# Performance work log

Measured on AMD Instinct MI355X. Metric: run time of the kernel, lower is better.

The kernel has to match this reference:

```python
import jax, jax.numpy as jnp
import numpy as np

N = 50000      # nodes
E = 800000     # edges
XS = 64        # x_size
ES = 32        # edge_attr dim (in_size = XS + ES = 96)
OUT = 64       # out_size
H = 128        # hidden_size
EPS = 1e-5


def _lin_init(k, fan_in, fan_out):
    s = 1.0 / np.sqrt(fan_in)
    kw, kb = jax.random.split(k)
    w = jax.random.uniform(kw, (fan_in, fan_out), minval=-s, maxval=s, dtype=jnp.float32)
    b = jax.random.uniform(kb, (fan_out,), minval=-s, maxval=s, dtype=jnp.float32)
    return w, b


def setup_inputs() -> dict:
    key = jax.random.key(0)
    ks = jax.random.split(key, 12)
    x = jax.random.normal(ks[0], (N, XS), dtype=jnp.float32)
    edge_index = jax.random.randint(ks[1], (2, E), 0, N, dtype=jnp.int64)
    edge_attr = jax.random.normal(ks[2], (E, ES), dtype=jnp.float32)
    u = jax.random.normal(ks[3], (1, 8), dtype=jnp.float32)
    batch = jnp.zeros((N,), dtype=jnp.int64)
    # MLP1: (96->128) LReLU (128->128) LReLU (128->64) LReLU LN(64)
    m1w0, m1b0 = _lin_init(ks[4], XS + ES, H)
    m1w1, m1b1 = _lin_init(ks[5], H, H)
    m1w2, m1b2 = _lin_init(ks[6], H, OUT)
    ln1_g = jnp.ones((OUT,), jnp.float32); ln1_b = jnp.zeros((OUT,), jnp.float32)
    # MLP2: (128->128) LReLU (128->128) LReLU (128->64) LReLU LN(64)
    m2w0, m2b0 = _lin_init(ks[7], XS + OUT, H)
    m2w1, m2b1 = _lin_init(ks[8], H, H)
    m2w2, m2b2 = _lin_init(ks[9], H, OUT)
    ln2_g = jnp.ones((OUT,), jnp.float32); ln2_b = jnp.zeros((OUT,), jnp.float32)
    return dict(x=x, edge_index=edge_index, edge_attr=edge_attr, u=u, batch=batch,
                m1w0=m1w0, m1b0=m1b0, m1w1=m1w1, m1b1=m1b1, m1w2=m1w2, m1b2=m1b2,
                ln1_g=ln1_g, ln1_b=ln1_b,
                m2w0=m2w0, m2b0=m2b0, m2w1=m2w1, m2b1=m2b1, m2w2=m2w2, m2b2=m2b2,
                ln2_g=ln2_g, ln2_b=ln2_b)


def _lrelu(v):
    return jax.nn.leaky_relu(v, 0.01)


def _layernorm(v, g, b):
    mu = jnp.mean(v, axis=-1, keepdims=True)
    var = jnp.mean(jnp.square(v - mu), axis=-1, keepdims=True)
    return (v - mu) * jax.lax.rsqrt(var + EPS) * g + b


def _mlp(h, w0, b0, w1, b1, w2, b2, g, bn):
    h = _lrelu(h @ w0 + b0)
    h = _lrelu(h @ w1 + b1)
    h = _lrelu(h @ w2 + b2)          # activate_last=True
    return _layernorm(h, g, bn)      # layer_norm=True


def reference(x, edge_index, edge_attr, u, batch,
              m1w0, m1b0, m1w1, m1b1, m1w2, m1b2, ln1_g, ln1_b,
              m2w0, m2b0, m2w1, m2b1, m2w2, m2b2, ln2_g, ln2_b):
    row, col = edge_index[0], edge_index[1]
    # gather source nodes, concat edge features -> per-edge MLP
    h = jnp.concatenate([x[row], edge_attr], axis=1)            # [E, 96]
    h = _mlp(h, m1w0, m1b0, m1w1, m1b1, m1w2, m1b2, ln1_g, ln1_b)  # [E, 64]
    # scatter_mean over destination nodes
    agg = jax.ops.segment_sum(h, col, num_segments=N)           # [N, 64]
    cnt = jax.ops.segment_sum(jnp.ones((E,), h.dtype), col, num_segments=N)
    agg = agg / jnp.maximum(cnt, 1.0)[:, None]
    # node update MLP
    h2 = jnp.concatenate([x, agg], axis=1)                      # [N, 128]
    return _mlp(h2, m2w0, m2b0, m2w1, m2b1, m2w2, m2b2, ln2_g, ln2_b)
```

## Files before the change

kernel.cpp:

```cpp
#include <hip/hip_runtime.h>


#define NNODES 50000
#define NEDGES 800000
#define NTILES_E 6250
#define NTILES_N 196

typedef __bf16 bf16;
typedef __bf16 __attribute__((ext_vector_type(4))) bf16x4;
typedef __bf16 __attribute__((ext_vector_type(8))) bf16x8;
typedef float __attribute__((ext_vector_type(4))) f32x4;

__device__ __forceinline__ f32x4 mfma_bf16(bf16x8 a, bf16x8 b, f32x4 c) {
    return __builtin_amdgcn_mfma_f32_16x16x32_bf16(a, b, c, 0, 0, 0);
}

__global__ void prep_weights(const float* __restrict__ w10, const float* __restrict__ w11,
                             const float* __restrict__ w12, const float* __restrict__ w20,
                             const float* __restrict__ w21, const float* __restrict__ w22,
                             bf16* __restrict__ img) {
    int idx = blockIdx.x * 256 + threadIdx.x;
    float f;
    if (idx < 13312) {
        int n = idx / 104, k = idx % 104;
        f = (k < 96) ? w10[k * 128 + n] : 0.0f;
    } else if (idx < 30720) {
        int t = idx - 13312; int n = t / 136, k = t % 136;
        f = (k < 128) ? w11[k * 128 + n] : 0.0f;
    } else if (idx < 39424) {
        int t = idx - 30720; int n = t / 136, k = t % 136;
        f = (k < 128) ? w12[k * 64 + n] : 0.0f;
    } else if (idx < 56832) {
        int t = idx - 39424; int n = t / 136, k = t % 136;
        f = (k < 128) ? w20[k * 128 + n] : 0.0f;
    } else if (idx < 74240) {
        int t = idx - 56832; int n = t / 136, k = t % 136;
        f = (k < 128) ? w21[k * 128 + n] : 0.0f;
    } else if (idx < 82944) {
        int t = idx - 74240; int n = t / 136, k = t % 136;
        f = (k < 128) ? w22[k * 64 + n] : 0.0f;
    } else {
        return;
    }
    img[idx] = (bf16)f;
}

__global__ void hist_kernel(const int* __restrict__ col, int* __restrict__ hist) {
    int i = blockIdx.x * 512 + threadIdx.x;
    if (i < NEDGES) {
        int d = col[i];
        if ((unsigned)d < (unsigned)NNODES) atomicAdd(hist + d, 1);
    }
}

__global__ void scanA(const int* __restrict__ hist, int* __restrict__ off,
                      int* __restrict__ csum) {
    __shared__ int sd[512];
    int t = threadIdx.x, i = blockIdx.x * 512 + t;
    int v = (i < NNODES) ? hist[i] : 0;
    sd[t] = v;
    __syncthreads();
    for (int o2 = 1; o2 < 512; o2 <<= 1) {
        int x = (t >= o2) ? sd[t - o2] : 0;
        __syncthreads();
        sd[t] += x;
        __syncthreads();
    }
    if (i < NNODES) off[i] = sd[t] - v;
    if (t == 511) csum[blockIdx.x] = sd[511];
}

__global__ void scanB(int* __restrict__ csum) {
    __shared__ int sd[128];
    int t = threadIdx.x;
    int v = (t < 98) ? csum[t] : 0;
    sd[t] = v;
    __syncthreads();
    for (int o2 = 1; o2 < 128; o2 <<= 1) {
        int x = (t >= o2) ? sd[t - o2] : 0;
        __syncthreads();
        sd[t] += x;
        __syncthreads();
    }
    if (t < 98) csum[t] = sd[t] - v;
}

__global__ void scanC(int* __restrict__ off, const int* __restrict__ csum) {
    int i = blockIdx.x * 512 + threadIdx.x;
    if (i < NNODES) off[i] += csum[blockIdx.x];
}

__global__ void scatter_kernel(const int* __restrict__ eidx, int* __restrict__ off,
                               int* __restrict__ perm, int* __restrict__ rdS) {
    int i = blockIdx.x * 512 + threadIdx.x;
    if (i < NEDGES) {
        int r = eidx[i], d = eidx[NEDGES + i];
        if ((unsigned)d < (unsigned)NNODES && (unsigned)r < (unsigned)NNODES) {
            int pos = atomicAdd(off + d, 1);
            if ((unsigned)pos < (unsigned)NEDGES) {
                perm[pos] = i;
                rdS[pos] = (int)(((unsigned)r & 0xFFFFu) | ((unsigned)d << 16));
            }
        }
    }
}

__global__ __launch_bounds__(256) void edge_mlp(
    const float* __restrict__ x, const int* __restrict__ perm,
    const int* __restrict__ rdS, const float* __restrict__ eattr,
    const bf16* __restrict__ wimg,
    const float* __restrict__ b0g, const float* __restrict__ b1g,
    const float* __restrict__ b2g, const float* __restrict__ lng,
    const float* __restrict__ lnb, float* __restrict__ agg) {
    __shared__ __align__(16) bf16 w1l[17408];
    __shared__ __align__(16) bf16 buf[128 * 136];
    __shared__ float bs[448];
    __shared__ int dstile[128];

    const int tid = threadIdx.x;
    {
        const uint4* src = (const uint4*)(wimg + 13312);
        uint4* dst = (uint4*)w1l;
        for (int i = tid; i < 2176; i += 256) dst[i] = src[i];
    }
    if (tid < 128) { bs[tid] = b0g[tid]; bs[128 + tid] = b1g[tid]; }
    else if (tid < 192) {
        int t = tid - 128;
        bs[256 + t] = b2g[t]; bs[320 + t] = lng[t]; bs[384 + t] = lnb[t];
    }
    __syncthreads();

    const int lane = tid & 63;
    const int wv = tid >> 6;
    const int col16 = lane & 15;
    const int quad = lane >> 4;

    float b0r[8], b1r[8], b2r[4], gr[4], br[4];
#pragma unroll
    for (int i = 0; i < 8; i++) { b0r[i] = bs[i * 16 + col16]; b1r[i] = bs[128 + i * 16 + col16]; }
#pragma unroll
    for (int i = 0; i < 4; i++) {
        b2r[i] = bs[256 + i * 16 + col16];
        gr[i] = bs[320 + i * 16 + col16];
        br[i] = bs[384 + i * 16 + col16];
    }

    const bf16* w0t = wimg;
    const bf16* w2t = wimg + 30720;

    const f32x4 vzero = {0.0f, 0.0f, 0.0f, 0.0f};
    const int r0 = wv * 32 + col16;
    const int rw = wv * 32 + quad * 4;
    const int el = tid >> 1, half = tid & 1;
    const int G = gridDim.x;

    int tile = blockIdx.x;

    float4 xr[8], er[4];
    unsigned cv;
    {
        int s = tile * 128 + el;
        cv = (unsigned)rdS[s];
        int ce = perm[s];
        int r = (int)(cv & 0xFFFFu); if (r >= NNODES) r = 0;
        if ((unsigned)ce >= (unsigned)NEDGES) ce = 0;
        const float4* xs = (const float4*)(x + (size_t)r * 64) + half * 8;
        const float4* es = (const float4*)(eattr + (size_t)ce * 32) + half * 4;
#pragma unroll
        for (int j = 0; j < 8; j++) xr[j] = xs[j];
#pragma unroll
        for (int j = 0; j < 4; j++) er[j] = es[j];
    }
    unsigned nv; int ne;
    {
        int t1 = tile + G;
        int s = (t1 < NTILES_E ? t1 * 128 : 0) + el;
        nv = (unsigned)rdS[s];
        ne = perm[s];
    }

    for (; tile < NTILES_E; tile += G) {
        {
            unsigned d = cv >> 16;
            if (half == 0) dstile[el] = (d < (unsigned)NNODES) ? (int)d : 0;
            bf16* arow = buf + el * 136;
#pragma unroll
            for (int j = 0; j < 8; j++) {
                float4 vv = xr[j];
                bf16x4 u = {(bf16)vv.x, (bf16)vv.y, (bf16)vv.z, (bf16)vv.w};
                *(bf16x4*)(arow + half * 32 + j * 4) = u;
            }
#pragma unroll
            for (int j = 0; j < 4; j++) {
                float4 vv = er[j];
                bf16x4 u = {(bf16)vv.x, (bf16)vv.y, (bf16)vv.z, (bf16)vv.w};
                *(bf16x4*)(arow + 64 + half * 16 + j * 4) = u;
            }
        }
        __syncthreads();

        {
            int t2 = tile + G;
            if (t2 < NTILES_E) {
                int r = (int)(nv & 0xFFFFu); if (r >= NNODES) r = 0;
                int e = ne; if ((unsigned)e >= (unsigned)NEDGES) e = 0;
                const float4* xs = (const float4*)(x + (size_t)r * 64) + half * 8;
                const float4* es = (const float4*)(eattr + (size_t)e * 32) + half * 4;
#pragma unroll
                for (int j = 0; j < 8; j++) xr[j] = xs[j];
#pragma unroll
                for (int j = 0; j < 4; j++) er[j] = es[j];
            }
        }
        unsigned pv; int pe;
        {
            int t3 = tile + 2 * G;
            int s = (t3 < NTILES_E ? t3 * 128 : 0) + el;
            pv = (unsigned)rdS[s];
            pe = perm[s];
        }

        f32x4 acc1[2][8];
#pragma unroll
        for (int mt = 0; mt < 2; mt++)
#pragma unroll
            for (int nt = 0; nt < 8; nt++) acc1[mt][nt] = vzero;
#pragma unroll
        for (int ks = 0; ks < 3; ks++) {
            bf16x8 a0 = *(const bf16x8*)(buf + r0 * 136 + ks * 32 + quad * 8);
            bf16x8 a1 = *(const bf16x8*)(buf + (r0 + 16) * 136 + ks * 32 + quad * 8);
#pragma unroll
            for (int nt = 0; nt < 8; nt++) {
                bf16x8 b = *(const bf16x8*)(w0t + (nt * 16 + col16) * 104 + ks * 32 + quad * 8);
                acc1[0][nt] = mfma_bf16(a0, b, acc1[0][nt]);
                acc1[1][nt] = mfma_bf16(a1, b, acc1[1][nt]);
            }
        }
#pragma unroll
        for (int mt = 0; mt < 2; mt++)
#pragma unroll
            for (int nt = 0; nt < 8; nt++)
#pragma unroll
                for (int rg = 0; rg < 4; rg++) {
                    float v = acc1[mt][nt][rg] + b0r[nt];
                    v = (v > 0.0f) ? v : 0.01f * v;
                    buf[(rw + mt * 16 + rg) * 136 + nt * 16 + col16] = (bf16)v;
                }

        bf16x8 a2[2][4];
#pragma unroll
        for (int mt = 0; mt < 2; mt++)
#pragma unroll
            for (int ks = 0; ks < 4; ks++)
                a2[mt][ks] = *(const bf16x8*)(buf + (r0 + mt * 16) * 136 + ks * 32 + quad * 8);
        f32x4 acc2[2][8];
#pragma unroll
        for (int mt = 0; mt < 2; mt++)
#pragma unroll
            for (int nt = 0; nt < 8; nt++) acc2[mt][nt] = vzero;
#pragma unroll
        for (int ks = 0; ks < 4; ks++) {
#pragma unroll
            for (int nt = 0; nt < 8; nt++) {
                bf16x8 b = *(const bf16x8*)(w1l + (nt * 16 + col16) * 136 + ks * 32 + quad * 8);
                acc2[0][nt] = mfma_bf16(a2[0][ks], b, acc2[0][nt]);
                acc2[1][nt] = mfma_bf16(a2[1][ks], b, acc2[1][nt]);
            }
        }
#pragma unroll
        for (int mt = 0; mt < 2; mt++)
#pragma unroll
            for (int nt = 0; nt < 8; nt++)
#pragma unroll
                for (int rg = 0; rg < 4; rg++) {
                    float v = acc2[mt][nt][rg] + b1r[nt];
                    v = (v > 0.0f) ? v : 0.01f * v;
                    buf[(rw + mt * 16 + rg) * 136 + nt * 16 + col16] = (bf16)v;
                }

        bf16x8 a3[2][4];
#pragma unroll
        for (int mt = 0; mt < 2; mt++)
#pragma unroll
            for (int ks = 0; ks < 4; ks++)
                a3[mt][ks] = *(const bf16x8*)(buf + (r0 + mt * 16) * 136 + ks * 32 + quad * 8);
        f32x4 acc3[2][4];
#pragma unroll
        for (int mt = 0; mt < 2; mt++)
#pragma unroll
            for (int nt = 0; nt < 4; nt++) acc3[mt][nt] = vzero;
#pragma unroll
        for (int ks = 0; ks < 4; ks++) {
#pragma unroll
            for (int nt = 0; nt < 4; nt++) {
                bf16x8 b = *(const bf16x8*)(w2t + (nt * 16 + col16) * 136 + ks * 32 + quad * 8);
                acc3[0][nt] = mfma_bf16(a3[0][ks], b, acc3[0][nt]);
                acc3[1][nt] = mfma_bf16(a3[1][ks], b, acc3[1][nt]);
            }
        }

        int drA[2][4];
#pragma unroll
        for (int mt = 0; mt < 2; mt++)
#pragma unroll
            for (int rg = 0; rg < 4; rg++) {
                int c = dstile[rw + mt * 16 + rg];
                drA[mt][rg] = ((unsigned)c < (unsigned)NNODES) ? c : 0;
            }
        __syncthreads();

#pragma unroll
        for (int mt = 0; mt < 2; mt++) {
            float vals[4][4];
            float s1[4] = {0.f, 0.f, 0.f, 0.f}, s2[4] = {0.f, 0.f, 0.f, 0.f};
#pragma unroll
            for (int nt = 0; nt < 4; nt++)
#pragma unroll
                for (int rg = 0; rg < 4; rg++) {
                    float v = acc3[mt][nt][rg] + b2r[nt];
                    v = (v > 0.0f) ? v : 0.01f * v;
                    vals[nt][rg] = v;
                    s1[rg] += v;
                    s2[rg] += v * v;
                }
#pragma unroll
            for (int off2 = 1; off2 < 16; off2 <<= 1) {
#pragma unroll
                for (int rg = 0; rg < 4; rg++) {
                    s1[rg] += __shfl_xor(s1[rg], off2);
                    s2[rg] += __shfl_xor(s2[rg], off2);
                }
            }
            float o[4][4];
#pragma unroll
            for (int rg = 0; rg < 4; rg++) {
                float mu = s1[rg] * 0.015625f;
                float var = s2[rg] * 0.015625f - mu * mu;
                float rstd = rsqrtf(var + 1e-5f);
#pragma unroll
                for (int nt = 0; nt < 4; nt++)
                    o[nt][rg] = (vals[nt][rg] - mu) * rstd * gr[nt] + br[nt];
            }
            float run0 = o[0][0], run1 = o[1][0], run2 = o[2][0], run3 = o[3][0];
            int cur = drA[mt][0];
#pragma unroll
            for (int rg = 1; rg < 4; rg++) {
                if (drA[mt][rg] != cur) {
                    float* dst = agg + (size_t)cur * 64 + col16;
                    atomicAdd(dst, run0); atomicAdd(dst + 16, run1);
                    atomicAdd(dst + 32, run2); atomicAdd(dst + 48, run3);
                    run0 = o[0][rg]; run1 = o[1][rg]; run2 = o[2][rg]; run3 = o[3][rg];
                    cur = drA[mt][rg];
                } else {
                    run0 += o[0][rg]; run1 += o[1][rg]; run2 += o[2][rg]; run3 += o[3][rg];
                }
            }
            float* dst = agg + (size_t)cur * 64 + col16;
            atomicAdd(dst, run0); atomicAdd(dst + 16, run1);
            atomicAdd(dst + 32, run2); atomicAdd(dst + 48, run3);
        }

        cv = nv; nv = pv; ne = pe;
    }
}

__global__ __launch_bounds__(512, 2) void node_mlp(
    const float* __restrict__ x, const float* __restrict__ agg,
    const int* __restrict__ hist, const bf16* __restrict__ wimg,
    const float* __restrict__ b0g, const float* __restrict__ b1g,
    const float* __restrict__ b2g, const float* __restrict__ lng,
    const float* __restrict__ lnb, float* __restrict__ out) {
    __shared__ __align__(16) bf16 wall[43520];
    __shared__ __align__(16) bf16 buf[256 * 136];
    __shared__ float bs[448];

    const int tid = threadIdx.x;
    {
        const uint4* src = (const uint4*)wimg;
        uint4* dst = (uint4*)wall;
        for (int i = tid; i < 5440; i += 512) dst[i] = src[i];
    }
    if (tid < 128) { bs[tid] = b0g[tid]; bs[128 + tid] = b1g[tid]; }
    else if (tid < 192) {
        int t = tid - 128;
        bs[256 + t] = b2g[t]; bs[320 + t] = lng[t]; bs[384 + t] = lnb[t];
    }
    __syncthreads();

    const int lane = tid & 63;
    const int wv = tid >> 6;
    const int col16 = lane & 15;
    const int quad = lane >> 4;

    float b0r[8], b1r[8], b2r[4], gr[4], br[4];
#pragma unroll
    for (int i = 0; i < 8; i++) { b0r[i] = bs[i * 16 + col16]; b1r[i] = bs[128 + i * 16 + col16]; }
#pragma unroll
    for (int i = 0; i < 4; i++) {
        b2r[i] = bs[256 + i * 16 + col16];
        gr[i] = bs[320 + i * 16 + col16];
        br[i] = bs[384 + i * 16 + col16];
    }

    const bf16* w0t = wall;
    const bf16* w1t = wall + 17408;
    const bf16* w2t = wall + 34816;

    const f32x4 vzero = {0.0f, 0.0f, 0.0f, 0.0f};
    const int r0 = wv * 32 + col16;
    const int rw = wv * 32 + quad * 4;
    const int el = tid >> 1, half = tid & 1;
    const int G = gridDim.x;

    int tile = blockIdx.x;
    if (tile >= NTILES_N) return;

    float4 xr[8], ar[8];
    int cc;
    {
        int i = tile * 256 + el;
        if (i >= NNODES) i = NNODES - 1;
        const float4* xs = (const float4*)(x + (size_t)i * 64) + half * 8;
        const float4* as = (const float4*)(agg + (size_t)i * 64) + half * 8;
#pragma unroll
        for (int j = 0; j < 8; j++) { xr[j] = xs[j]; ar[j] = as[j]; }
        cc = hist[i];
    }

    for (; tile < NTILES_N; tile += G) {
        const int nbase = tile * 256;
        {
            float inv = 1.0f / (float)(cc > 1 ? cc : 1);
            bf16* arow = buf + el * 136;
#pragma unroll
            for (int j = 0; j < 8; j++) {
                float4 v = xr[j];
                bf16x4 u = {(bf16)v.x, (bf16)v.y, (bf16)v.z, (bf16)v.w};
                *(bf16x4*)(arow + half * 32 + j * 4) = u;
            }
#pragma unroll
            for (int j = 0; j < 8; j++) {
                float4 v = ar[j];
                bf16x4 u = {(bf16)(v.x * inv), (bf16)(v.y * inv), (bf16)(v.z * inv), (bf16)(v.w * inv)};
                *(bf16x4*)(arow + 64 + half * 32 + j * 4) = u;
            }
        }
        __syncthreads();

        {
            int t2 = tile + G;
            if (t2 < NTILES_N) {
                int i = t2 * 256 + el;
                if (i >= NNODES) i = NNODES - 1;
                const float4* xs = (const float4*)(x + (size_t)i * 64) + half * 8;
                const float4* as = (const float4*)(agg + (size_t)i * 64) + half * 8;
#pragma unroll
                for (int j = 0; j < 8; j++) { xr[j] = xs[j]; ar[j] = as[j]; }
                cc = hist[i];
            }
        }

        f32x4 acc1[2][8];
#pragma unroll
        for (int mt = 0; mt < 2; mt++)
#pragma unroll
            for (int nt = 0; nt < 8; nt++) acc1[mt][nt] = vzero;
#pragma unroll
        for (int ks = 0; ks < 4; ks++) {
            bf16x8 a0 = *(const bf16x8*)(buf + r0 * 136 + ks * 32 + quad * 8);
            bf16x8 a1 = *(const bf16x8*)(buf + (r0 + 16) * 136 + ks * 32 + quad * 8);
#pragma unroll
            for (int nt = 0; nt < 8; nt++) {
                bf16x8 b = *(const bf16x8*)(w0t + (nt * 16 + col16) * 136 + ks * 32 + quad * 8);
                acc1[0][nt] = mfma_bf16(a0, b, acc1[0][nt]);
                acc1[1][nt] = mfma_bf16(a1, b, acc1[1][nt]);
            }
        }
#pragma unroll
        for (int mt = 0; mt < 2; mt++)
#pragma unroll
            for (int nt = 0; nt < 8; nt++)
#pragma unroll
                for (int rg = 0; rg < 4; rg++) {
                    float v = acc1[mt][nt][rg] + b0r[nt];
                    v = (v > 0.0f) ? v : 0.01f * v;
                    buf[(rw + mt * 16 + rg) * 136 + nt * 16 + col16] = (bf16)v;
                }

        bf16x8 a2[2][4];
#pragma unroll
        for (int mt = 0; mt < 2; mt++)
#pragma unroll
            for (int ks = 0; ks < 4; ks++)
                a2[mt][ks] = *(const bf16x8*)(buf + (r0 + mt * 16) * 136 + ks * 32 + quad * 8);
        f32x4 acc2[2][8];
#pragma unroll
        for (int mt = 0; mt < 2; mt++)
#pragma unroll
            for (int nt = 0; nt < 8; nt++) acc2[mt][nt] = vzero;
#pragma unroll
        for (int ks = 0; ks < 4; ks++) {
#pragma unroll
            for (int nt = 0; nt < 8; nt++) {
                bf16x8 b = *(const bf16x8*)(w1t + (nt * 16 + col16) * 136 + ks * 32 + quad * 8);
                acc2[0][nt] = mfma_bf16(a2[0][ks], b, acc2[0][nt]);
                acc2[1][nt] = mfma_bf16(a2[1][ks], b, acc2[1][nt]);
            }
        }
#pragma unroll
        for (int mt = 0; mt < 2; mt++)
#pragma unroll
            for (int nt = 0; nt < 8; nt++)
#pragma unroll
                for (int rg = 0; rg < 4; rg++) {
                    float v = acc2[mt][nt][rg] + b1r[nt];
                    v = (v > 0.0f) ? v : 0.01f * v;
                    buf[(rw + mt * 16 + rg) * 136 + nt * 16 + col16] = (bf16)v;
                }

        bf16x8 a3[2][4];
#pragma unroll
        for (int mt = 0; mt < 2; mt++)
#pragma unroll
            for (int ks = 0; ks < 4; ks++)
                a3[mt][ks] = *(const bf16x8*)(buf + (r0 + mt * 16) * 136 + ks * 32 + quad * 8);
        f32x4 acc3[2][4];
#pragma unroll
        for (int mt = 0; mt < 2; mt++)
#pragma unroll
            for (int nt = 0; nt < 4; nt++) acc3[mt][nt] = vzero;
#pragma unroll
        for (int ks = 0; ks < 4; ks++) {
#pragma unroll
            for (int nt = 0; nt < 4; nt++) {
                bf16x8 b = *(const bf16x8*)(w2t + (nt * 16 + col16) * 136 + ks * 32 + quad * 8);
                acc3[0][nt] = mfma_bf16(a3[0][ks], b, acc3[0][nt]);
                acc3[1][nt] = mfma_bf16(a3[1][ks], b, acc3[1][nt]);
            }
        }
        __syncthreads();

#pragma unroll
        for (int mt = 0; mt < 2; mt++) {
            float vals[4][4];
            float s1[4] = {0.f, 0.f, 0.f, 0.f}, s2[4] = {0.f, 0.f, 0.f, 0.f};
#pragma unroll
            for (int nt = 0; nt < 4; nt++)
#pragma unroll
                for (int rg = 0; rg < 4; rg++) {
                    float v = acc3[mt][nt][rg] + b2r[nt];
                    v = (v > 0.0f) ? v : 0.01f * v;
                    vals[nt][rg] = v;
                    s1[rg] += v;
                    s2[rg] += v * v;
                }
#pragma unroll
            for (int off2 = 1; off2 < 16; off2 <<= 1) {
#pragma unroll
                for (int rg = 0; rg < 4; rg++) {
                    s1[rg] += __shfl_xor(s1[rg], off2);
                    s2[rg] += __shfl_xor(s2[rg], off2);
                }
            }
#pragma unroll
            for (int rg = 0; rg < 4; rg++) {
                float mu = s1[rg] * 0.015625f;
                float var = s2[rg] * 0.015625f - mu * mu;
                float rstd = rsqrtf(var + 1e-5f);
                int i = nbase + rw + mt * 16 + rg;
                if (i < NNODES) {
#pragma unroll
                    for (int nt = 0; nt < 4; nt++) {
                        float o = (vals[nt][rg] - mu) * rstd * gr[nt] + br[nt];
                        out[(size_t)i * 64 + nt * 16 + col16] = o;
                    }
                }
            }
        }
    }
}

extern "C" void kernel_launch(void* const* d_in, const int* in_sizes, int n_in,
                              void* d_out, int out_size, void* d_ws, size_t ws_size,
                              hipStream_t stream) {
    (void)in_sizes; (void)n_in; (void)out_size; (void)ws_size;
    const float* x     = (const float*)d_in[0];
    const int*   eidx  = (const int*)d_in[1];
    const float* eattr = (const float*)d_in[2];
    const float* m1w0 = (const float*)d_in[5];
    const float* m1b0 = (const float*)d_in[6];
    const float* m1w1 = (const float*)d_in[7];
    const float* m1b1 = (const float*)d_in[8];
    const float* m1w2 = (const float*)d_in[9];
    const float* m1b2 = (const float*)d_in[10];
    const float* ln1g = (const float*)d_in[11];
    const float* ln1b = (const float*)d_in[12];
    const float* m2w0 = (const float*)d_in[13];
    const float* m2b0 = (const float*)d_in[14];
    const float* m2w1 = (const float*)d_in[15];
    const float* m2b1 = (const float*)d_in[16];
    const float* m2w2 = (const float*)d_in[17];
    const float* m2b2 = (const float*)d_in[18];
    const float* ln2g = (const float*)d_in[19];
    const float* ln2b = (const float*)d_in[20];

    char* ws = (char*)d_ws;
    float* agg  = (float*)ws;
    int*   hist = (int*)(ws + 12800000);
    int*   off  = (int*)(ws + 13000000);
    int*   csum = (int*)(ws + 13200000);
    int*   perm = (int*)(ws + 13200512);
    int*   rdS  = (int*)(ws + 16400512);
    bf16*  wimg = (bf16*)(ws + 19600512);

    hipMemsetAsync(d_ws, 0, 13000000, stream);
    prep_weights<<<324, 256, 0, stream>>>(m1w0, m1w1, m1w2, m2w0, m2w1, m2w2, wimg);
    hist_kernel<<<1563, 512, 0, stream>>>(eidx + NEDGES, hist);
    scanA<<<98, 512, 0, stream>>>(hist, off, csum);
    scanB<<<1, 128, 0, stream>>>(csum);
    scanC<<<98, 512, 0, stream>>>(off, csum);
    scatter_kernel<<<1563, 512, 0, stream>>>(eidx, off, perm, rdS);
    edge_mlp<<<512, 256, 0, stream>>>(x, perm, rdS, eattr, wimg,
                                      m1b0, m1b1, m1b2, ln1g, ln1b, agg);
    node_mlp<<<196, 512, 0, stream>>>(x, agg, hist, wimg + 39424,
                                      m2b0, m2b1, m2b2, ln2g, ln2b, (float*)d_out);
}
```

Measured before the change: 512.1 us.

## Merge scan phases and read layer-1 weights from global instead of LDS

```diff
diff --git a/kernel.cpp b/kernel.cpp
--- a/kernel.cpp
+++ b/kernel.cpp
@@ -70,24 +70,20 @@
     if (t == 511) csum[blockIdx.x] = sd[511];
 }
 
-__global__ void scanB(int* __restrict__ csum) {
-    __shared__ int sd[128];
+__global__ void scanC(int* __restrict__ off, const int* __restrict__ csum) {
+    __shared__ int sbc;
     int t = threadIdx.x;
-    int v = (t < 98) ? csum[t] : 0;
-    sd[t] = v;
+    if (t < 64) {
+        int p = 0;
+        for (int j = t; j < (int)blockIdx.x; j += 64) p += csum[j];
+#pragma unroll
+        for (int o = 32; o > 0; o >>= 1) p += __shfl_down(p, o);
+        if (t == 0) sbc = p;
+    }
     __syncthreads();
-    for (int o2 = 1; o2 < 128; o2 <<= 1) {
-        int x = (t >= o2) ? sd[t - o2] : 0;
-        __syncthreads();
-        sd[t] += x;
-        __syncthreads();
-    }
-    if (t < 98) csum[t] = sd[t] - v;
-}
-
-__global__ void scanC(int* __restrict__ off, const int* __restrict__ csum) {
-    int i = blockIdx.x * 512 + threadIdx.x;
-    if (i < NNODES) off[i] += csum[blockIdx.x];
+    int pre = sbc;
+    int i = blockIdx.x * 512 + t;
+    if (i < NNODES) off[i] += pre;
 }
 
 __global__ void scatter_kernel(const int* __restrict__ eidx, int* __restrict__ off,
@@ -112,17 +108,11 @@
     const float* __restrict__ b0g, const float* __restrict__ b1g,
     const float* __restrict__ b2g, const float* __restrict__ lng,
     const float* __restrict__ lnb, float* __restrict__ agg) {
-    __shared__ __align__(16) bf16 w1l[17408];
     __shared__ __align__(16) bf16 buf[128 * 136];
     __shared__ float bs[448];
     __shared__ int dstile[128];
 
     const int tid = threadIdx.x;
-    {
-        const uint4* src = (const uint4*)(wimg + 13312);
-        uint4* dst = (uint4*)w1l;
-        for (int i = tid; i < 2176; i += 256) dst[i] = src[i];
-    }
     if (tid < 128) { bs[tid] = b0g[tid]; bs[128 + tid] = b1g[tid]; }
     else if (tid < 192) {
         int t = tid - 128;
@@ -146,6 +136,7 @@
     }
 
     const bf16* w0t = wimg;
+    const bf16* w1t = wimg + 13312;
     const bf16* w2t = wimg + 30720;
 
     const f32x4 vzero = {0.0f, 0.0f, 0.0f, 0.0f};
@@ -262,7 +253,7 @@
         for (int ks = 0; ks < 4; ks++) {
 #pragma unroll
             for (int nt = 0; nt < 8; nt++) {
-                bf16x8 b = *(const bf16x8*)(w1l + (nt * 16 + col16) * 136 + ks * 32 + quad * 8);
+                bf16x8 b = *(const bf16x8*)(w1t + (nt * 16 + col16) * 136 + ks * 32 + quad * 8);
                 acc2[0][nt] = mfma_bf16(a2[0][ks], b, acc2[0][nt]);
                 acc2[1][nt] = mfma_bf16(a2[1][ks], b, acc2[1][nt]);
             }
@@ -617,7 +608,6 @@
     prep_weights<<<324, 256, 0, stream>>>(m1w0, m1w1, m1w2, m2w0, m2w1, m2w2, wimg);
     hist_kernel<<<1563, 512, 0, stream>>>(eidx + NEDGES, hist);
     scanA<<<98, 512, 0, stream>>>(hist, off, csum);
-    scanB<<<1, 128, 0, stream>>>(csum);
     scanC<<<98, 512, 0, stream>>>(off, csum);
     scatter_kernel<<<1563, 512, 0, stream>>>(eidx, off, perm, rdS);
     edge_mlp<<<512, 256, 0, stream>>>(x, perm, rdS, eattr, wimg,
```

Result: slower. 558.6 us (+9.1%).
